# Kernel tuning notes

Hardware: AMD Instinct MI355X
Metric: run time of the kernel (lower is better)

Reference implementation:

```python
import jax, jax.numpy as jnp
import numpy as np

EPS = 1e-5

def _bn2d(x, gamma, beta):
    # training-mode BatchNorm2d: stats over (B, T, F) per channel, biased var
    m = x.mean(axis=(0, 2, 3), keepdims=True)
    v = x.var(axis=(0, 2, 3), keepdims=True)
    return (x - m) * jax.lax.rsqrt(v + EPS) * gamma[None, :, None, None] + beta[None, :, None, None]

def _gn1(x, gamma, beta):
    # GroupNorm(num_groups=1) on (B, C, T): stats over (C, T) per sample
    m = x.mean(axis=(1, 2), keepdims=True)
    v = x.var(axis=(1, 2), keepdims=True)
    return (x - m) * jax.lax.rsqrt(v + EPS) * gamma[None, :, None] + beta[None, :, None]

def _nearest(x, size):
    # torch F.interpolate(mode='nearest') on last dim: src = floor(dst * L_in / L_out)
    L = x.shape[-1]
    idx = jnp.floor(jnp.arange(size) * (L / size)).astype(jnp.int32)
    return x[..., idx]


def setup_inputs() -> dict:
    key = jax.random.key(0)
    ks = jax.random.split(key, 16)
    B, Ca, T, Fa = 2, 512, 256, 128
    Tv = 64
    d = {
        "audio": jax.random.normal(ks[0], (B, Ca, T, Fa), dtype=jnp.float32),
        "video_emb": jax.random.normal(ks[1], (B, Ca, Tv), dtype=jnp.float32),
        # value_conv: depthwise 1x1 Conv2d (no bias) + BatchNorm2d
        "value_w": jax.random.normal(ks[2], (Ca,), dtype=jnp.float32) * 0.1 + 1.0,
        "value_gamma": jax.random.normal(ks[3], (Ca,), dtype=jnp.float32) * 0.1 + 1.0,
        "value_beta": jax.random.normal(ks[4], (Ca,), dtype=jnp.float32) * 0.1,
        # gate_conv: depthwise 1x1 Conv2d (no bias) + BatchNorm2d + ReLU
        "gate_w": jax.random.normal(ks[5], (Ca,), dtype=jnp.float32) * 0.1 + 1.0,
        "gate_gamma": jax.random.normal(ks[6], (Ca,), dtype=jnp.float32) * 0.1 + 1.0,
        "gate_beta": jax.random.normal(ks[7], (Ca,), dtype=jnp.float32) * 0.1,
        # attention_conv: depthwise Conv1d (bias) + GroupNorm(1)
        "att_w": jax.random.normal(ks[8], (Ca,), dtype=jnp.float32) * 0.1 + 1.0,
        "att_b": jax.random.normal(ks[9], (Ca,), dtype=jnp.float32) * 0.1,
        "att_gamma": jax.random.normal(ks[10], (Ca,), dtype=jnp.float32) * 0.1 + 1.0,
        "att_beta": jax.random.normal(ks[11], (Ca,), dtype=jnp.float32) * 0.1,
        # resize_conv: depthwise Conv1d (bias) + GroupNorm(1)
        "res_w": jax.random.normal(ks[12], (Ca,), dtype=jnp.float32) * 0.1 + 1.0,
        "res_b": jax.random.normal(ks[13], (Ca,), dtype=jnp.float32) * 0.1,
        "res_gamma": jax.random.normal(ks[14], (Ca,), dtype=jnp.float32) * 0.1 + 1.0,
        "res_beta": jax.random.normal(ks[15], (Ca,), dtype=jnp.float32) * 0.1,
    }
    return d


def reference(audio, video_emb, value_w, value_gamma, value_beta,
              gate_w, gate_gamma, gate_beta,
              att_w, att_b, att_gamma, att_beta,
              res_w, res_b, res_gamma, res_beta):
    T = audio.shape[2]
    # value branch: depthwise 1x1 conv (per-channel scale) + BN
    a_v = _bn2d(audio * value_w[None, :, None, None], value_gamma, value_beta)  # (B,Ca,T,Fa)
    # attention from video: depthwise conv1d + GN(1) + softmax over time + nearest resize
    att = _gn1(video_emb * att_w[None, :, None] + att_b[None, :, None], att_gamma, att_beta)
    att = _nearest(jax.nn.softmax(att, axis=-1), T)  # (B,Ca,T)
    f1 = att[..., None] * a_v
    # gating branch
    vr = _gn1(video_emb * res_w[None, :, None] + res_b[None, :, None], res_gamma, res_beta)
    vi = _nearest(vr, T)[..., None]  # (B,Ca,T,1)
    a_gate = jax.nn.relu(_bn2d(audio * gate_w[None, :, None, None], gate_gamma, gate_beta))
    f2 = a_gate * vi
    return f1 + f2
```

## Files before the change

kernel.cpp:

```cpp
#include <hip/hip_runtime.h>
#include <math.h>

#define EPS 1e-5f

typedef float f32x4 __attribute__((ext_vector_type(4)));

constexpr int B   = 2;
constexpr int Ca  = 512;
constexpr int T   = 256;
constexpr int Fa  = 128;
constexpr int Tv  = 64;
constexpr int CHW = T * Fa;
constexpr int NSTAT = B * CHW;
constexpr int VID_PER_B = Ca * Tv;

constexpr int WS_PS   = 0;
constexpr int WS_PS2  = 2048;
constexpr int WS_ATT  = 4096;
constexpr int WS_VR   = WS_ATT + B * VID_PER_B;

__global__ __launch_bounds__(256) void k_pre(
    const float* __restrict__ audio,
    const float* __restrict__ video,
    const float* __restrict__ aw, const float* __restrict__ ab,
    const float* __restrict__ ag, const float* __restrict__ abeta,
    const float* __restrict__ rw, const float* __restrict__ rb,
    const float* __restrict__ rg, const float* __restrict__ rbeta,
    float* __restrict__ ws)
{
    const int blk = blockIdx.x;
    const int tid = threadIdx.x;
    __shared__ float sh[17];

    if (blk < 2048) {
        const f32x4* a4 = reinterpret_cast<const f32x4*>(audio) + (size_t)blk * 4096;
        float s = 0.f, s2 = 0.f;
        #pragma unroll
        for (int k = 0; k < 16; ++k) {
            f32x4 v = a4[tid + k * 256];
            s  += v.x + v.y + v.z + v.w;
            s2 += v.x * v.x + v.y * v.y + v.z * v.z + v.w * v.w;
        }
        for (int off = 32; off; off >>= 1) {
            s  += __shfl_xor(s,  off);
            s2 += __shfl_xor(s2, off);
        }
        const int wid = tid >> 6;
        if ((tid & 63) == 0) { sh[wid] = s; sh[4 + wid] = s2; }
        __syncthreads();
        if (tid == 0) {
            ws[WS_PS  + blk] = sh[0] + sh[1] + sh[2] + sh[3];
            ws[WS_PS2 + blk] = sh[4] + sh[5] + sh[6] + sh[7];
        }
        return;
    }

    const int b  = blk - 2048;
    const int t  = tid & 63;
    const int cl = tid >> 6;
    const float* vbase = video + (size_t)b * VID_PER_B;
    float* att_out = ws + WS_ATT;
    float* vr_out  = ws + WS_VR;

    float s1a = 0.f, s2a = 0.f, s1r = 0.f, s2r = 0.f;
    #pragma unroll 8
    for (int i = 0; i < Ca / 4; ++i) {
        const int c = cl + 4 * i;
        float v  = vbase[c * Tv + t];
        float xa = v * aw[c] + ab[c];
        float xr = v * rw[c] + rb[c];
        s1a += xa; s2a += xa * xa;
        s1r += xr; s2r += xr * xr;
    }
    for (int off = 32; off; off >>= 1) {
        s1a += __shfl_xor(s1a, off); s2a += __shfl_xor(s2a, off);
        s1r += __shfl_xor(s1r, off); s2r += __shfl_xor(s2r, off);
    }
    const int wid = tid >> 6;
    if ((tid & 63) == 0) {
        sh[wid]      = s1a; sh[4 + wid]  = s2a;
        sh[8 + wid]  = s1r; sh[12 + wid] = s2r;
    }
    __syncthreads();
    if (tid == 0) {
        float S1a = sh[0] + sh[1] + sh[2] + sh[3];
        float S2a = sh[4] + sh[5] + sh[6] + sh[7];
        float S1r = sh[8] + sh[9] + sh[10] + sh[11];
        float S2r = sh[12] + sh[13] + sh[14] + sh[15];
        const float inv = 1.f / (float)VID_PER_B;
        float ma = S1a * inv, va = S2a * inv - ma * ma;
        float mr = S1r * inv, vv = S2r * inv - mr * mr;
        sh[0] = ma; sh[1] = rsqrtf(va + EPS);
        sh[2] = mr; sh[3] = rsqrtf(vv + EPS);
    }
    __syncthreads();
    const float ma = sh[0], rsa = sh[1];
    const float mr = sh[2], rsr = sh[3];

    #pragma unroll 8
    for (int i = 0; i < Ca / 4; ++i) {
        const int c = cl + 4 * i;
        float v  = vbase[c * Tv + t];
        float xa = (v * aw[c] + ab[c] - ma) * rsa * ag[c] + abeta[c];
        float xr = (v * rw[c] + rb[c] - mr) * rsr * rg[c] + rbeta[c];

        float m = xa;
        for (int off = 32; off; off >>= 1) m = fmaxf(m, __shfl_xor(m, off));
        float e = expf(xa - m);
        float sum = e;
        for (int off = 32; off; off >>= 1) sum += __shfl_xor(sum, off);

        const size_t idx = (size_t)b * VID_PER_B + (size_t)c * Tv + t;
        att_out[idx] = e / sum;
        vr_out[idx]  = xr;
    }
}

__global__ __launch_bounds__(256) void k_fuse(
    const float* __restrict__ audio,
    const float* __restrict__ ws,
    const float* __restrict__ vw, const float* __restrict__ vg, const float* __restrict__ vb,
    const float* __restrict__ gw, const float* __restrict__ gg, const float* __restrict__ gb,
    float* __restrict__ out)
{
    const int blk = blockIdx.x;
    const int tid = threadIdx.x;
    const f32x4* a4 = reinterpret_cast<const f32x4*>(audio);
    f32x4*       o4 = reinterpret_cast<f32x4*>(out);

    const size_t bc = (size_t)(blk >> 3);
    const int    c  = (int)(bc & (size_t)(Ca - 1));
    const int    t_base = (blk & 7) * 32;

    const float* ps  = ws + WS_PS;
    const float* ps2 = ws + WS_PS2;
    const float S  = ps[c * 2]  + ps[c * 2 + 1]  + ps[1024 + c * 2]  + ps[1024 + c * 2 + 1];
    const float S2 = ps2[c * 2] + ps2[c * 2 + 1] + ps2[1024 + c * 2] + ps2[1024 + c * 2 + 1];
    const float inv  = 1.f / (float)NSTAT;
    const float mean = S * inv;
    const float var  = S2 * inv - mean * mean;
    float w  = vw[c];
    const float sv = w * rsqrtf(w * w * var + EPS) * vg[c];
    const float bv = vb[c] - mean * sv;
    w = gw[c];
    const float sg = w * rsqrtf(w * w * var + EPS) * gg[c];
    const float bg = gb[c] - mean * sg;

    const float* att = ws + WS_ATT + bc * Tv;
    const float* vr  = ws + WS_VR  + bc * Tv;

    #pragma unroll
    for (int k = 0; k < 4; ++k) {
        const size_t i = (size_t)blk * 1024 + tid + (size_t)k * 256;
        const int    t = t_base + k * 8 + (tid >> 5);
        const float av = att[t >> 2];
        const float vv = vr[t >> 2];

        f32x4 a = __builtin_nontemporal_load(&a4[i]);
        f32x4 r;
        r.x = av * (a.x * sv + bv) + fmaxf(a.x * sg + bg, 0.f) * vv;
        r.y = av * (a.y * sv + bv) + fmaxf(a.y * sg + bg, 0.f) * vv;
        r.z = av * (a.z * sv + bv) + fmaxf(a.z * sg + bg, 0.f) * vv;
        r.w = av * (a.w * sv + bv) + fmaxf(a.w * sg + bg, 0.f) * vv;
        __builtin_nontemporal_store(r, &o4[i]);
    }
}

extern "C" void kernel_launch(void* const* d_in, const int* in_sizes, int n_in,
                              void* d_out, int out_size, void* d_ws, size_t ws_size,
                              hipStream_t stream) {
    const float* audio   = (const float*)d_in[0];
    const float* video   = (const float*)d_in[1];
    const float* value_w = (const float*)d_in[2];
    const float* value_g = (const float*)d_in[3];
    const float* value_b = (const float*)d_in[4];
    const float* gate_w  = (const float*)d_in[5];
    const float* gate_g  = (const float*)d_in[6];
    const float* gate_b  = (const float*)d_in[7];
    const float* att_w   = (const float*)d_in[8];
    const float* att_b   = (const float*)d_in[9];
    const float* att_g   = (const float*)d_in[10];
    const float* att_be  = (const float*)d_in[11];
    const float* res_w   = (const float*)d_in[12];
    const float* res_b   = (const float*)d_in[13];
    const float* res_g   = (const float*)d_in[14];
    const float* res_be  = (const float*)d_in[15];

    float* ws = (float*)d_ws;

    k_pre<<<2050, 256, 0, stream>>>(audio, video,
                                    att_w, att_b, att_g, att_be,
                                    res_w, res_b, res_g, res_be, ws);
    const int blocks = B * Ca * T * Fa / 4 / 1024;
    k_fuse<<<blocks, 256, 0, stream>>>(audio, ws,
                                       value_w, value_g, value_b,
                                       gate_w, gate_g, gate_b,
                                       (float*)d_out);
}
```

Baseline: 323.9 us.

## Move video softmax and GN application into fuse kernel, vectorize video stats

The pre kernel now only computes the GroupNorm mean and rstd for the video embedding, reading it with vectorized float4 loads, and writes four scalars per batch. Each fuse block recomputes its channel's 64-element attention softmax and resize values from the raw video into shared memory. The two video blocks previously did a long serial normalize-and-softmax tail while the rest of the GPU waited, and that tail is removed. In exchange every fuse block does a small redundant softmax plus a barrier, and the audio load switches from nontemporal to a normal load.

```diff
diff --git a/kernel.cpp b/kernel.cpp
--- a/kernel.cpp
+++ b/kernel.cpp
@@ -16,21 +16,18 @@
 
 constexpr int WS_PS   = 0;
 constexpr int WS_PS2  = 2048;
-constexpr int WS_ATT  = 4096;
-constexpr int WS_VR   = WS_ATT + B * VID_PER_B;
+constexpr int WS_VID  = 4096;
 
 __global__ __launch_bounds__(256) void k_pre(
     const float* __restrict__ audio,
     const float* __restrict__ video,
     const float* __restrict__ aw, const float* __restrict__ ab,
-    const float* __restrict__ ag, const float* __restrict__ abeta,
     const float* __restrict__ rw, const float* __restrict__ rb,
-    const float* __restrict__ rg, const float* __restrict__ rbeta,
     float* __restrict__ ws)
 {
     const int blk = blockIdx.x;
     const int tid = threadIdx.x;
-    __shared__ float sh[17];
+    __shared__ float sh[16];
 
     if (blk < 2048) {
         const f32x4* a4 = reinterpret_cast<const f32x4*>(audio) + (size_t)blk * 4096;
@@ -55,22 +52,24 @@
         return;
     }
 
-    const int b  = blk - 2048;
-    const int t  = tid & 63;
-    const int cl = tid >> 6;
-    const float* vbase = video + (size_t)b * VID_PER_B;
-    float* att_out = ws + WS_ATT;
-    float* vr_out  = ws + WS_VR;
+    const int b = blk - 2048;
+    const f32x4* v4 = reinterpret_cast<const f32x4*>(video) + (size_t)b * (VID_PER_B / 4);
 
     float s1a = 0.f, s2a = 0.f, s1r = 0.f, s2r = 0.f;
     #pragma unroll 8
-    for (int i = 0; i < Ca / 4; ++i) {
-        const int c = cl + 4 * i;
-        float v  = vbase[c * Tv + t];
-        float xa = v * aw[c] + ab[c];
-        float xr = v * rw[c] + rb[c];
-        s1a += xa; s2a += xa * xa;
-        s1r += xr; s2r += xr * xr;
+    for (int j = 0; j < VID_PER_B / 4 / 256; ++j) {
+        const int q = tid + j * 256;
+        const int c = q >> 4;
+        const float wa = aw[c], ba = ab[c];
+        const float wr = rw[c], br = rb[c];
+        f32x4 v = v4[q];
+        #pragma unroll
+        for (int e = 0; e < 4; ++e) {
+            float xa = v[e] * wa + ba;
+            float xr = v[e] * wr + br;
+            s1a += xa; s2a += xa * xa;
+            s1r += xr; s2r += xr * xr;
+        }
     }
     for (int off = 32; off; off >>= 1) {
         s1a += __shfl_xor(s1a, off); s2a += __shfl_xor(s2a, off);
@@ -90,46 +89,35 @@
         const float inv = 1.f / (float)VID_PER_B;
         float ma = S1a * inv, va = S2a * inv - ma * ma;
         float mr = S1r * inv, vv = S2r * inv - mr * mr;
-        sh[0] = ma; sh[1] = rsqrtf(va + EPS);
-        sh[2] = mr; sh[3] = rsqrtf(vv + EPS);
-    }
-    __syncthreads();
-    const float ma = sh[0], rsa = sh[1];
-    const float mr = sh[2], rsr = sh[3];
-
-    #pragma unroll 8
-    for (int i = 0; i < Ca / 4; ++i) {
-        const int c = cl + 4 * i;
-        float v  = vbase[c * Tv + t];
-        float xa = (v * aw[c] + ab[c] - ma) * rsa * ag[c] + abeta[c];
-        float xr = (v * rw[c] + rb[c] - mr) * rsr * rg[c] + rbeta[c];
-
-        float m = xa;
-        for (int off = 32; off; off >>= 1) m = fmaxf(m, __shfl_xor(m, off));
-        float e = expf(xa - m);
-        float sum = e;
-        for (int off = 32; off; off >>= 1) sum += __shfl_xor(sum, off);
-
-        const size_t idx = (size_t)b * VID_PER_B + (size_t)c * Tv + t;
-        att_out[idx] = e / sum;
-        vr_out[idx]  = xr;
+        ws[WS_VID + b * 4 + 0] = ma;
+        ws[WS_VID + b * 4 + 1] = rsqrtf(va + EPS);
+        ws[WS_VID + b * 4 + 2] = mr;
+        ws[WS_VID + b * 4 + 3] = rsqrtf(vv + EPS);
     }
 }
 
 __global__ __launch_bounds__(256) void k_fuse(
     const float* __restrict__ audio,
+    const float* __restrict__ video,
     const float* __restrict__ ws,
     const float* __restrict__ vw, const float* __restrict__ vg, const float* __restrict__ vb,
     const float* __restrict__ gw, const float* __restrict__ gg, const float* __restrict__ gb,
+    const float* __restrict__ aw, const float* __restrict__ ab,
+    const float* __restrict__ ag, const float* __restrict__ abeta,
+    const float* __restrict__ rw, const float* __restrict__ rb,
+    const float* __restrict__ rg, const float* __restrict__ rbeta,
     float* __restrict__ out)
 {
     const int blk = blockIdx.x;
     const int tid = threadIdx.x;
     const f32x4* a4 = reinterpret_cast<const f32x4*>(audio);
     f32x4*       o4 = reinterpret_cast<f32x4*>(out);
+    __shared__ float sm_att[Tv];
+    __shared__ float sm_vr[Tv];
 
     const size_t bc = (size_t)(blk >> 3);
     const int    c  = (int)(bc & (size_t)(Ca - 1));
+    const int    b  = (int)(bc >> 9);
     const int    t_base = (blk & 7) * 32;
 
     const float* ps  = ws + WS_PS;
@@ -146,17 +134,34 @@
     const float sg = w * rsqrtf(w * w * var + EPS) * gg[c];
     const float bg = gb[c] - mean * sg;
 
-    const float* att = ws + WS_ATT + bc * Tv;
-    const float* vr  = ws + WS_VR  + bc * Tv;
+    if (tid < 64) {
+        const int t = tid;
+        const float ma  = ws[WS_VID + b * 4 + 0];
+        const float rsa = ws[WS_VID + b * 4 + 1];
+        const float mr  = ws[WS_VID + b * 4 + 2];
+        const float rsr = ws[WS_VID + b * 4 + 3];
+        const float v = video[(size_t)b * VID_PER_B + (size_t)c * Tv + t];
+        const float xa = (v * aw[c] + ab[c] - ma) * rsa * ag[c] + abeta[c];
+        const float xr = (v * rw[c] + rb[c] - mr) * rsr * rg[c] + rbeta[c];
+
+        float m = xa;
+        for (int off = 32; off; off >>= 1) m = fmaxf(m, __shfl_xor(m, off));
+        float e = expf(xa - m);
+        float sum = e;
+        for (int off = 32; off; off >>= 1) sum += __shfl_xor(sum, off);
+        sm_att[t] = e / sum;
+        sm_vr[t]  = xr;
+    }
+    __syncthreads();
 
     #pragma unroll
     for (int k = 0; k < 4; ++k) {
         const size_t i = (size_t)blk * 1024 + tid + (size_t)k * 256;
         const int    t = t_base + k * 8 + (tid >> 5);
-        const float av = att[t >> 2];
-        const float vv = vr[t >> 2];
-
-        f32x4 a = __builtin_nontemporal_load(&a4[i]);
+        const float av = sm_att[t >> 2];
+        const float vv = sm_vr[t >> 2];
+
+        f32x4 a = a4[i];
         f32x4 r;
         r.x = av * (a.x * sv + bv) + fmaxf(a.x * sg + bg, 0.f) * vv;
         r.y = av * (a.y * sv + bv) + fmaxf(a.y * sg + bg, 0.f) * vv;
@@ -188,12 +193,12 @@
 
     float* ws = (float*)d_ws;
 
-    k_pre<<<2050, 256, 0, stream>>>(audio, video,
-                                    att_w, att_b, att_g, att_be,
-                                    res_w, res_b, res_g, res_be, ws);
+    k_pre<<<2050, 256, 0, stream>>>(audio, video, att_w, att_b, res_w, res_b, ws);
     const int blocks = B * Ca * T * Fa / 4 / 1024;
-    k_fuse<<<blocks, 256, 0, stream>>>(audio, ws,
+    k_fuse<<<blocks, 256, 0, stream>>>(audio, video, ws,
                                        value_w, value_g, value_b,
                                        gate_w, gate_g, gate_b,
+                                       att_w, att_b, att_g, att_be,
+                                       res_w, res_b, res_g, res_be,
                                        (float*)d_out);
 }
```

After: 288.3 us. 11.0% less time.
